# Kernel optimization log

Measured on AMD Instinct MI355X. Metric: run time of the kernel, lower is better.

## Reference

```python
import jax, jax.numpy as jnp
import numpy as np

B, N, IN, H, K, D, L = 8, 1024, 32, 32, 3, 16, 2  # batch, nodes, input_dim, hidden, cheb_k, embed_dim, layers


def setup_inputs() -> dict:
    key = jax.random.key(0)
    ks = jax.random.split(key, 4 + 4 * L)
    inp = {
        "xt": jax.random.normal(ks[0], (B, N, IN), jnp.float32),
        "init_state": jax.random.normal(ks[1], (L, B, N, H), jnp.float32),
        # row-normalized-ish support so the Chebyshev recursion stays bounded
        "support": jax.random.uniform(ks[2], (N, N), jnp.float32) / N,
        "embeddings": jax.random.normal(ks[3], (B, N, D), jnp.float32),
    }
    i = 4
    for l in range(L):
        cin = IN if l == 0 else H
        gi = K * (cin + H)
        inp[f"gate_w{l}"] = jax.random.normal(ks[i], (D, gi, 2 * H), jnp.float32) * (2.0 / (gi + 2 * H)) ** 0.5; i += 1
        inp[f"gate_b{l}"] = jax.random.normal(ks[i], (D, 2 * H), jnp.float32) * 0.05; i += 1
        inp[f"upd_w{l}"] = jax.random.normal(ks[i], (D, gi, H), jnp.float32) * (2.0 / (gi + H)) ** 0.5; i += 1
        inp[f"upd_b{l}"] = jax.random.normal(ks[i], (D, H), jnp.float32) * 0.05; i += 1
    return inp


def _cheb_gconv(x, support, emb, w_pool, b_pool):
    """HimGCN_share forward, meta_axis='ST', 2-D support.
    x: [B,N,C]; support: [N,N]; emb: [B,N,D];
    w_pool: [D, K*C, O]; b_pool: [D, O]. Returns [B,N,O]."""
    n = support.shape[0]
    graphs = [jnp.eye(n, dtype=x.dtype), support]
    for _ in range(2, K):
        graphs.append(2.0 * support @ graphs[-1] - graphs[-2])
    G = jnp.stack(graphs)                                   # [K,N,N]
    c = x.shape[-1]
    x_g = jnp.einsum('knm,bmc->bnkc', G, x).reshape(x.shape[0], n, K * c)  # concat over k
    # faithful to einsum('bni,bnio->bno') with bnio = einsum('bnd,dio->bnio'),
    # contracted in a memory-lighter order (same math)
    xe = jnp.einsum('bni,bnd->bnid', x_g, emb)              # [B,N,K*C,D]
    out = jnp.einsum('bnid,dio->bno', xe, w_pool)
    out = out + jnp.einsum('bnd,do->bno', emb, b_pool)
    return out


def _gcru_cell(x, state, support, emb, gw, gb, uw, ub):
    inp = jnp.concatenate([x, state], axis=-1)
    z_r = jax.nn.sigmoid(_cheb_gconv(inp, support, emb, gw, gb))
    z, r = z_r[..., :H], z_r[..., H:]
    cand = jnp.concatenate([x, z * state], axis=-1)
    hc = jnp.tanh(_cheb_gconv(cand, support, emb, uw, ub))
    return r * state + (1.0 - r) * hc


def reference(xt, init_state, support, embeddings,
              gate_w0, gate_b0, upd_w0, upd_b0,
              gate_w1, gate_b1, upd_w1, upd_b1):
    params = [(gate_w0, gate_b0, upd_w0, upd_b0), (gate_w1, gate_b1, upd_w1, upd_b1)]
    cur = xt
    hidden = []
    for l in range(L):
        gw, gb, uw, ub = params[l]
        cur = _gcru_cell(cur, init_state[l], support, embeddings, gw, gb, uw, ub)
        hidden.append(cur)
    return cur, jnp.stack(hidden)
```

## Files before the change

kernel.cpp:

```cpp
#include <hip/hip_runtime.h>
#include <math.h>

#define BB 8
#define NN 1024
#define HH 32
#define II 192
#define DD 16
#define BN (BB*NN)
#define MT 16
#define FR 512

typedef __attribute__((ext_vector_type(8))) short short8v;
typedef __attribute__((ext_vector_type(4))) float float4v;

union Frag8 { short8v v; uint2 u[2]; uint4 q; };

static __device__ inline ushort bf(float x) {
  union { float f; unsigned u; } c; c.f = x;
  unsigned r = c.u + 0x7FFFu + ((c.u >> 16) & 1u);
  return (ushort)(r >> 16);
}

static __device__ inline uint4 pack8(const ushort e[8]) {
  uint4 v;
  v.x = (unsigned)e[0] | ((unsigned)e[1] << 16);
  v.y = (unsigned)e[2] | ((unsigned)e[3] << 16);
  v.z = (unsigned)e[4] | ((unsigned)e[5] << 16);
  v.w = (unsigned)e[6] | ((unsigned)e[7] << 16);
  return v;
}

template <int O>
static __device__ void prep_w_frag(const float* __restrict__ W,
                                   ushort* __restrict__ WF, int d,
                                   float* lds)
{
  constexpr int NCG = O / 16;
  const float* Wd = W + (size_t)d * II * O;
  ushort* WFd = WF + (size_t)d * NCG * 6 * FR;
  const int tid = threadIdx.x;
  for (int f = tid; f < II * O / 4; f += 256) {
    int i = f / (O / 4);
    int o4 = (f % (O / 4)) * 4;
    float4 v = *(const float4*)(Wd + (size_t)i * O + o4);
    lds[i * (O + 1) + o4 + 0] = v.x; lds[i * (O + 1) + o4 + 1] = v.y;
    lds[i * (O + 1) + o4 + 2] = v.z; lds[i * (O + 1) + o4 + 3] = v.w;
  }
  __syncthreads();
  for (int f = tid; f < NCG * 6 * 64; f += 256) {
    int rem = f % 384;
    int ks = rem >> 6, l = rem & 63;
    int o = (f / 384) * 16 + (l & 15);
    int kb = ks * 32 + (l >> 4) * 4;
    ushort e[8];
#pragma unroll
    for (int j = 0; j < 4; ++j) {
      e[j] = bf(lds[(kb + j) * (O + 1) + o]);
      e[4 + j] = bf(lds[(kb + 16 + j) * (O + 1) + o]);
    }
    *(uint4*)(WFd + (size_t)f * 8) = pack8(e);
  }
}

__global__ __launch_bounds__(256) void prep_all(
    const float* __restrict__ S,
    ushort* __restrict__ SbF, ushort* __restrict__ S2bF,
    const float* __restrict__ gw0, const float* __restrict__ gw1,
    ushort* __restrict__ wfg0, ushort* __restrict__ wfg1,
    const float* __restrict__ uw0, const float* __restrict__ uw1,
    ushort* __restrict__ wfu0, ushort* __restrict__ wfu1,
    const float* __restrict__ xt, const float* __restrict__ st0,
    const float* __restrict__ st1,
    ushort* __restrict__ xbTFg0, ushort* __restrict__ xbTFg1)
{
  union PrepSm {
    float wlds[II * 65];
    struct { ushort A[32][136]; ushort Bt[32][132]; ushort C2[32][36]; } s2;
    ushort T[32 * 72];
  };
  __shared__ PrepSm sm;
  int bx = blockIdx.x;
  const int tid = threadIdx.x;

  if (bx < 1024) {
    const int m0 = (bx >> 5) * 32, n0 = (bx & 31) * 32;
    const int w = tid >> 6, l = tid & 63;
    const int l15 = l & 15, l4 = l >> 4;
    const int wr = (w & 1) * 16, wc = (w >> 1) * 16;

    float4v acc = (float4v){0.f, 0.f, 0.f, 0.f};
    for (int k0 = 0; k0 < NN; k0 += 128) {
      __syncthreads();
#pragma unroll
      for (int q = 0; q < 2; ++q) {
        int f = tid + q * 256;
        int row = f >> 4, s8 = (f & 15) * 8;
        float4 lo = *(const float4*)(S + (size_t)(m0 + row) * NN + k0 + s8);
        float4 hi = *(const float4*)(S + (size_t)(m0 + row) * NN + k0 + s8 + 4);
        sm.s2.A[row][s8 + 0] = bf(lo.x); sm.s2.A[row][s8 + 1] = bf(lo.y);
        sm.s2.A[row][s8 + 2] = bf(lo.z); sm.s2.A[row][s8 + 3] = bf(lo.w);
        sm.s2.A[row][s8 + 4] = bf(hi.x); sm.s2.A[row][s8 + 5] = bf(hi.y);
        sm.s2.A[row][s8 + 6] = bf(hi.z); sm.s2.A[row][s8 + 7] = bf(hi.w);
      }
#pragma unroll
      for (int q = 0; q < 2; ++q) {
        int u = tid + q * 256;
        int kp = u >> 3, c4 = (u & 7) * 4;
        float4 a = *(const float4*)(S + (size_t)(k0 + 2 * kp) * NN + n0 + c4);
        float4 b = *(const float4*)(S + (size_t)(k0 + 2 * kp + 1) * NN + n0 + c4);
        *(unsigned*)&sm.s2.Bt[c4 + 0][2 * kp] = (unsigned)bf(a.x) | ((unsigned)bf(b.x) << 16);
        *(unsigned*)&sm.s2.Bt[c4 + 1][2 * kp] = (unsigned)bf(a.y) | ((unsigned)bf(b.y) << 16);
        *(unsigned*)&sm.s2.Bt[c4 + 2][2 * kp] = (unsigned)bf(a.z) | ((unsigned)bf(b.z) << 16);
        *(unsigned*)&sm.s2.Bt[c4 + 3][2 * kp] = (unsigned)bf(a.w) | ((unsigned)bf(b.w) << 16);
      }
      __syncthreads();
#pragma unroll
      for (int ks = 0; ks < 4; ++ks) {
        int kb = ks * 32 + l4 * 4;
        Frag8 af, bfr;
        af.u[0] = *(const uint2*)&sm.s2.A[wr + l15][kb];
        af.u[1] = *(const uint2*)&sm.s2.A[wr + l15][kb + 16];
        bfr.u[0] = *(const uint2*)&sm.s2.Bt[wc + l15][kb];
        bfr.u[1] = *(const uint2*)&sm.s2.Bt[wc + l15][kb + 16];
        acc = __builtin_amdgcn_mfma_f32_16x16x32_bf16(af.v, bfr.v, acc, 0, 0, 0);
      }
    }
    __syncthreads();
#pragma unroll
    for (int r = 0; r < 4; ++r)
      sm.s2.C2[wr + l4 * 4 + r][wc + l15] = bf(2.f * acc[r]);
    __syncthreads();
    if (tid < 128) {
      int fh = tid >> 6, l2 = tid & 63;
      ushort e[8];
#pragma unroll
      for (int j = 0; j < 4; ++j) {
        e[j] = sm.s2.C2[fh * 16 + (l2 & 15)][(l2 >> 4) * 4 + j];
        e[4 + j] = sm.s2.C2[fh * 16 + (l2 & 15)][(l2 >> 4) * 4 + 16 + j];
      }
      *(uint4*)(S2bF + ((size_t)((bx >> 5) * 2 + fh) * 32 + (bx & 31)) * FR +
                (size_t)l2 * 8) = pack8(e);
    }
    return;
  }
  bx -= 1024;
  if (bx < 32) {
    prep_w_frag<64>(bx >= 16 ? gw1 : gw0, bx >= 16 ? wfg1 : wfg0, bx & 15,
                    sm.wlds);
    return;
  }
  bx -= 32;
  if (bx < 32) {
    prep_w_frag<32>(bx >= 16 ? uw1 : uw0, bx >= 16 ? wfu1 : wfu0, bx & 15,
                    sm.wlds);
    return;
  }
  bx -= 32;
  if (bx < 384) {
    const int tensor = bx / 128, seg = bx % 128;
    const float* src = tensor == 0 ? xt : (tensor == 1 ? st0 : st1);
    ushort* T = sm.T;
    const int n0 = seg * 64;
#pragma unroll
    for (int q = 0; q < 2; ++q) {
      int f = tid + q * 256;
      int n = f >> 3, c4 = (f & 7) * 4;
      float4 v = *(const float4*)(src + (size_t)(n0 + n) * 32 + c4);
      T[(c4 + 0) * 72 + n] = bf(v.x); T[(c4 + 1) * 72 + n] = bf(v.y);
      T[(c4 + 2) * 72 + n] = bf(v.z); T[(c4 + 3) * 72 + n] = bf(v.w);
    }
    __syncthreads();
    {
      int gg = tid >> 7, ksl = (tid >> 6) & 1, l = tid & 63;
      int c = gg * 16 + (l & 15);
      int nb = ksl * 32 + (l >> 4) * 4;
      ushort e[8];
#pragma unroll
      for (int j = 0; j < 4; ++j) {
        e[j] = T[c * 72 + nb + j];
        e[4 + j] = T[c * 72 + nb + 16 + j];
      }
      int b = seg >> 4;
      int ks = (seg & 15) * 2 + ksl;
      ushort* dst; int g;
      if (tensor == 0)      { dst = xbTFg0; g = gg; }
      else if (tensor == 1) { dst = xbTFg0; g = 2 + gg; }
      else                  { dst = xbTFg1; g = 2 + gg; }
      *(uint4*)(dst + (((size_t)b * 4 + g) * 32 + ks) * FR + (size_t)l * 8) =
          pack8(e);
    }
    return;
  }
  bx -= 384;
  {
    const int mt = bx;
#pragma unroll
    for (int q = 0; q < 8; ++q) {
      int f = tid + q * 256;
      int ks = f >> 6, l = f & 63;
      int row = mt * 16 + (l & 15);
      int kb = ks * 32 + (l >> 4) * 4;
      float4 lo = *(const float4*)(S + (size_t)row * NN + kb);
      float4 hi = *(const float4*)(S + (size_t)row * NN + kb + 16);
      ushort e[8] = {bf(lo.x), bf(lo.y), bf(lo.z), bf(lo.w),
                     bf(hi.x), bf(hi.y), bf(hi.z), bf(hi.w)};
      *(uint4*)(SbF + ((size_t)mt * 32 + ks) * FR + (size_t)l * 8) = pack8(e);
    }
  }
}

template <int PHASE>
__global__ __launch_bounds__(256) void gconv_fused(
    const float* __restrict__ xb1,
    const float* __restrict__ xb2,
    const ushort* __restrict__ xbTF,
    const ushort* __restrict__ SbF,
    const ushort* __restrict__ S2bF,
    const float* __restrict__ emb,
    const ushort* __restrict__ WF,
    const float* __restrict__ bias,
    ushort* __restrict__ gT1c,
    float* __restrict__ gT2c,
    float* __restrict__ zr,
    float* __restrict__ zs,
    const float* __restrict__ state,
    float* __restrict__ hid,
    float* __restrict__ outp,
    ushort* __restrict__ xbTFout)
{
  constexpr int O = PHASE == 0 ? 64 : 32;
  constexpr int NCG = O / 16;
  __shared__ ushort A_sm[MT][200];
  __shared__ float emb_sm[MT][17];
  __shared__ float bias_sm[16][64];

  const int bid = blockIdx.x;
  const int mt = (bid & 7) * 8 + ((bid >> 3) & 7);
  const int b = bid >> 6;
  const int m0 = mt * MT;
  const int tid = threadIdx.x;
  const int w = tid >> 6, l = tid & 63;
  const int l15 = l & 15, l4 = l >> 4;
  const int wcp = (PHASE == 0) ? w * 16 : (w & 1) * 16;

  if (tid < MT * 4) {
    int row = tid >> 2, d4 = (tid & 3) * 4;
    float4 v = *(const float4*)(emb + ((size_t)b * NN + m0 + row) * DD + d4);
    emb_sm[row][d4 + 0] = v.x; emb_sm[row][d4 + 1] = v.y;
    emb_sm[row][d4 + 2] = v.z; emb_sm[row][d4 + 3] = v.w;
  }
  for (int f = tid; f < DD * O / 4; f += 256) {
    int d = f / (O / 4), o4 = (f % (O / 4)) * 4;
    *(float4*)&bias_sm[d][o4] = *(const float4*)(bias + (size_t)d * O + o4);
  }
  {
    int row = tid >> 4, c4 = (tid & 15) * 4;
    const float* src = (c4 < 32) ? xb1 : xb2;
    float4 v = *(const float4*)(src + ((size_t)b * NN + m0 + row) * 32 + (c4 & 31));
    ushort4 o; o.x = bf(v.x); o.y = bf(v.y); o.z = bf(v.z); o.w = bf(v.w);
    *(ushort4*)&A_sm[row][c4] = o;
  }

  float4v acc1 = (float4v){0.f, 0.f, 0.f, 0.f};
  float4v acc2 = (float4v){0.f, 0.f, 0.f, 0.f};
  {
    const ushort* a1p = SbF + (size_t)mt * 32 * FR + (size_t)l * 8;
    const ushort* a2p = S2bF + (size_t)mt * 32 * FR + (size_t)l * 8;
    const ushort* bp = xbTF +
        (((size_t)b * NCG + (PHASE == 0 ? w : (w & 1))) * 32) * FR +
        (size_t)l * 8;
#pragma unroll 4
    for (int ks = 0; ks < 32; ++ks) {
      Frag8 a1, a2, b0;
      a1.q = *(const uint4*)(a1p + (size_t)ks * FR);
      a2.q = *(const uint4*)(a2p + (size_t)ks * FR);
      b0.q = *(const uint4*)(bp + (size_t)ks * FR);
      acc1 = __builtin_amdgcn_mfma_f32_16x16x32_bf16(a1.v, b0.v, acc1, 0, 0, 0);
      acc2 = __builtin_amdgcn_mfma_f32_16x16x32_bf16(a2.v, b0.v, acc2, 0, 0, 0);
    }
  }

  if (PHASE == 0 && w < 2) {
#pragma unroll
    for (int r = 0; r < 4; ++r) {
      size_t m = (size_t)b * NN + m0 + l4 * 4 + r;
      gT1c[m * 32 + wcp + l15] = bf(acc1[r]);
      gT2c[m * 32 + wcp + l15] = acc2[r];
    }
  }

  if (PHASE == 1) {
#pragma unroll
    for (int q = 0; q < 2; ++q) {
      int e = tid + q * 256;
      int row = e >> 5, c = e & 31;
      size_t m = (size_t)b * NN + m0 + row;
      A_sm[row][64 + c] = gT1c[m * 32 + c];
      A_sm[row][128 + c] = bf(gT2c[m * 32 + c] - xb1[m * 32 + c]);
    }
  }
  {
    const int colX = (PHASE == 0 ? 0 : 32) + wcp + l15;
    if (PHASE == 0 || w < 2) {
#pragma unroll
      for (int r = 0; r < 4; ++r) {
        int row = l4 * 4 + r;
        const float* src = (colX < 32) ? xb1 : xb2;
        float xv = src[((size_t)b * NN + m0 + row) * 32 + (colX & 31)];
        A_sm[row][64 + colX] = bf(acc1[r]);
        A_sm[row][128 + colX] = bf(acc2[r] - xv);
      }
    }
  }
  __syncthreads();

  const int cg = (PHASE == 0) ? w : (w & 1);
  const int ocol = cg * 16 + l15;
  const int erow = l4 * 4;
  const ushort* wfp = WF + (size_t)cg * 6 * FR + (size_t)l * 8;

  float4v outacc = (float4v){0.f, 0.f, 0.f, 0.f};

#pragma unroll 2
  for (int d = 0; d < DD; ++d) {
    const ushort* wpd = wfp + (size_t)d * NCG * 6 * FR;
    float4v acc = (float4v){0.f, 0.f, 0.f, 0.f};
#pragma unroll
    for (int ks = 0; ks < 6; ++ks) {
      int kb = ks * 32 + l4 * 4;
      Frag8 af, bfr;
      af.u[0] = *(const uint2*)&A_sm[l15][kb];
      af.u[1] = *(const uint2*)&A_sm[l15][kb + 16];
      bfr.q = *(const uint4*)(wpd + (size_t)ks * FR);
      acc = __builtin_amdgcn_mfma_f32_16x16x32_bf16(af.v, bfr.v, acc, 0, 0, 0);
    }
    float bb = bias_sm[d][ocol];
    outacc[0] += emb_sm[erow + 0][d] * (acc[0] + bb);
    outacc[1] += emb_sm[erow + 1][d] * (acc[1] + bb);
    outacc[2] += emb_sm[erow + 2][d] * (acc[2] + bb);
    outacc[3] += emb_sm[erow + 3][d] * (acc[3] + bb);
  }

  const int ksn = m0 >> 5;
  const int ebase = (m0 & 16) ? 4 : 0;
  const int lanep = l4 * 16 + (ocol & 15);

  if (PHASE == 0) {
    float zss[4];
#pragma unroll
    for (int r = 0; r < 4; ++r) {
      size_t m = (size_t)b * NN + m0 + erow + r;
      float zv = 1.f / (1.f + __expf(-outacc[r]));
      zr[m * 64 + ocol] = zv;
      if (ocol < 32) {
        float sv = zv * xb2[m * 32 + ocol];
        zs[m * 32 + ocol] = sv;
        zss[r] = sv;
      }
    }
    if (ocol < 32) {
      ushort4 pk; pk.x = bf(zss[0]); pk.y = bf(zss[1]);
      pk.z = bf(zss[2]); pk.w = bf(zss[3]);
      *(ushort4*)(xbTFout + (((size_t)b * 2 + (ocol >> 4)) * 32 + ksn) * FR +
                  (size_t)lanep * 8 + ebase) = pk;
    }
  } else if (w < 2) {
    float res[4];
#pragma unroll
    for (int r = 0; r < 4; ++r) {
      size_t m = (size_t)b * NN + m0 + erow + r;
      float hc = tanhf(outacc[r]);
      float rg = zr[m * 64 + 32 + ocol];
      float st = state[m * 32 + ocol];
      res[r] = rg * st + (1.f - rg) * hc;
      hid[m * 32 + ocol] = res[r];
      if (outp) outp[m * 32 + ocol] = res[r];
    }
    if (xbTFout) {
      ushort4 pk; pk.x = bf(res[0]); pk.y = bf(res[1]);
      pk.z = bf(res[2]); pk.w = bf(res[3]);
      *(ushort4*)(xbTFout + (((size_t)b * 4 + (ocol >> 4)) * 32 + ksn) * FR +
                  (size_t)lanep * 8 + ebase) = pk;
    }
  }
}

extern "C" void kernel_launch(void* const* d_in, const int* in_sizes, int n_in,
                              void* d_out, int out_size, void* d_ws, size_t ws_size,
                              hipStream_t stream)
{
  const float* xt         = (const float*)d_in[0];
  const float* init_state = (const float*)d_in[1];
  const float* S          = (const float*)d_in[2];
  const float* emb        = (const float*)d_in[3];

  float* out    = (float*)d_out;
  float* hidden = out + (size_t)BN * HH;

  float* zr   = (float*)d_ws;
  float* zs   = zr + (size_t)BN * 64;
  float* gT2c = zs + (size_t)BN * 32;
  ushort* gT1c = (ushort*)(gT2c + (size_t)BN * 32);
  ushort* SbF  = gT1c + (size_t)BN * 32;
  ushort* S2bF = SbF + (size_t)NN * NN;
  ushort* wfg0 = S2bF + (size_t)NN * NN;
  ushort* wfu0 = wfg0 + (size_t)DD * 4 * 6 * FR;
  ushort* wfg1 = wfu0 + (size_t)DD * 2 * 6 * FR;
  ushort* wfu1 = wfg1 + (size_t)DD * 4 * 6 * FR;
  ushort* xbTFg0 = wfu1 + (size_t)DD * 2 * 6 * FR;
  ushort* xbTFu0 = xbTFg0 + (size_t)BB * 4 * 32 * FR;
  ushort* xbTFg1 = xbTFu0 + (size_t)BB * 2 * 32 * FR;
  ushort* xbTFu1 = xbTFg1 + (size_t)BB * 4 * 32 * FR;

  const float* st0 = init_state;
  const float* st1 = init_state + (size_t)BN * HH;
  float* hid0 = hidden;
  float* hid1 = hidden + (size_t)BN * HH;

  prep_all<<<1536, 256, 0, stream>>>(
      S, SbF, S2bF,
      (const float*)d_in[4], (const float*)d_in[8], wfg0, wfg1,
      (const float*)d_in[6], (const float*)d_in[10], wfu0, wfu1,
      xt, st0, st1, xbTFg0, xbTFg1);

  gconv_fused<0><<<512, 256, 0, stream>>>(
      xt, st0, xbTFg0, SbF, S2bF, emb, wfg0, (const float*)d_in[5],
      gT1c, gT2c, zr, zs, nullptr, nullptr, nullptr, xbTFu0);
  gconv_fused<1><<<512, 256, 0, stream>>>(
      xt, zs, xbTFu0, SbF, S2bF, emb, wfu0, (const float*)d_in[7],
      gT1c, gT2c, zr, nullptr, st0, hid0, nullptr, xbTFg1);
  gconv_fused<0><<<512, 256, 0, stream>>>(
      hid0, st1, xbTFg1, SbF, S2bF, emb, wfg1, (const float*)d_in[9],
      gT1c, gT2c, zr, zs, nullptr, nullptr, nullptr, xbTFu1);
  gconv_fused<1><<<512, 256, 0, stream>>>(
      hid0, zs, xbTFu1, SbF, S2bF, emb, wfu1, (const float*)d_in[11],
      gT1c, gT2c, zr, nullptr, st1, hid1, out, nullptr);
}
```

Baseline: 99.87 us.

## Split-K gconv across two wave groups with LDS reduction, 512 threads

Doubles the block to 512 threads. The second group of four waves handles the other half of the K loop in the graph-propagation GEMM and the other half of the embedding dimension loop, and the partial results are reduced through a new shared-memory buffer. This halves the serial MFMA chain per wave and raises the number of waves in flight, since the grid has only 512 blocks. The cost is two extra barriers, more LDS traffic and larger shared-memory use per block. The phase-1 loads of gT1c/gT2c are also moved earlier so they overlap with the first GEMM.

Result: faster. 94.87 us (-5.0%).

```diff
diff --git a/kernel.cpp b/kernel.cpp
--- a/kernel.cpp
+++ b/kernel.cpp
@@ -210,7 +210,7 @@
 }
 
 template <int PHASE>
-__global__ __launch_bounds__(256) void gconv_fused(
+__global__ __launch_bounds__(512) void gconv_fused(
     const float* __restrict__ xb1,
     const float* __restrict__ xb2,
     const ushort* __restrict__ xbTF,
@@ -233,6 +233,7 @@
   __shared__ ushort A_sm[MT][200];
   __shared__ float emb_sm[MT][17];
   __shared__ float bias_sm[16][64];
+  __shared__ float red_sm[4][64][9];
 
   const int bid = blockIdx.x;
   const int mt = (bid & 7) * 8 + ((bid >> 3) & 7);
@@ -240,8 +241,9 @@
   const int m0 = mt * MT;
   const int tid = threadIdx.x;
   const int w = tid >> 6, l = tid & 63;
+  const int cw = w & 3, kh = w >> 2;
   const int l15 = l & 15, l4 = l >> 4;
-  const int wcp = (PHASE == 0) ? w * 16 : (w & 1) * 16;
+  const int wcp = (PHASE == 0) ? cw * 16 : (cw & 1) * 16;
 
   if (tid < MT * 4) {
     int row = tid >> 2, d4 = (tid & 3) * 4;
@@ -249,16 +251,22 @@
     emb_sm[row][d4 + 0] = v.x; emb_sm[row][d4 + 1] = v.y;
     emb_sm[row][d4 + 2] = v.z; emb_sm[row][d4 + 3] = v.w;
   }
-  for (int f = tid; f < DD * O / 4; f += 256) {
+  for (int f = tid; f < DD * O / 4; f += 512) {
     int d = f / (O / 4), o4 = (f % (O / 4)) * 4;
     *(float4*)&bias_sm[d][o4] = *(const float4*)(bias + (size_t)d * O + o4);
   }
-  {
+  if (tid < 256) {
     int row = tid >> 4, c4 = (tid & 15) * 4;
     const float* src = (c4 < 32) ? xb1 : xb2;
     float4 v = *(const float4*)(src + ((size_t)b * NN + m0 + row) * 32 + (c4 & 31));
     ushort4 o; o.x = bf(v.x); o.y = bf(v.y); o.z = bf(v.z); o.w = bf(v.w);
     *(ushort4*)&A_sm[row][c4] = o;
+  }
+  if (PHASE == 1) {
+    int row = tid >> 5, c = tid & 31;
+    size_t m = (size_t)b * NN + m0 + row;
+    A_sm[row][64 + c] = gT1c[m * 32 + c];
+    A_sm[row][128 + c] = bf(gT2c[m * 32 + c] - xb1[m * 32 + c]);
   }
 
   float4v acc1 = (float4v){0.f, 0.f, 0.f, 0.f};
@@ -267,10 +275,10 @@
     const ushort* a1p = SbF + (size_t)mt * 32 * FR + (size_t)l * 8;
     const ushort* a2p = S2bF + (size_t)mt * 32 * FR + (size_t)l * 8;
     const ushort* bp = xbTF +
-        (((size_t)b * NCG + (PHASE == 0 ? w : (w & 1))) * 32) * FR +
+        (((size_t)b * NCG + (PHASE == 0 ? cw : (cw & 1))) * 32) * FR +
         (size_t)l * 8;
 #pragma unroll 4
-    for (int ks = 0; ks < 32; ++ks) {
+    for (int ks = kh * 16; ks < kh * 16 + 16; ++ks) {
       Frag8 a1, a2, b0;
       a1.q = *(const uint4*)(a1p + (size_t)ks * FR);
       a2.q = *(const uint4*)(a2p + (size_t)ks * FR);
@@ -280,28 +288,30 @@
     }
   }
 
-  if (PHASE == 0 && w < 2) {
-#pragma unroll
-    for (int r = 0; r < 4; ++r) {
-      size_t m = (size_t)b * NN + m0 + l4 * 4 + r;
-      gT1c[m * 32 + wcp + l15] = bf(acc1[r]);
-      gT2c[m * 32 + wcp + l15] = acc2[r];
-    }
-  }
-
-  if (PHASE == 1) {
-#pragma unroll
-    for (int q = 0; q < 2; ++q) {
-      int e = tid + q * 256;
-      int row = e >> 5, c = e & 31;
-      size_t m = (size_t)b * NN + m0 + row;
-      A_sm[row][64 + c] = gT1c[m * 32 + c];
-      A_sm[row][128 + c] = bf(gT2c[m * 32 + c] - xb1[m * 32 + c]);
-    }
-  }
-  {
-    const int colX = (PHASE == 0 ? 0 : 32) + wcp + l15;
-    if (PHASE == 0 || w < 2) {
+  if (kh == 1) {
+#pragma unroll
+    for (int j = 0; j < 4; ++j) {
+      red_sm[cw][l][j] = acc1[j];
+      red_sm[cw][l][4 + j] = acc2[j];
+    }
+  }
+  __syncthreads();
+  if (kh == 0) {
+#pragma unroll
+    for (int j = 0; j < 4; ++j) {
+      acc1[j] += red_sm[cw][l][j];
+      acc2[j] += red_sm[cw][l][4 + j];
+    }
+    if (PHASE == 0 && cw < 2) {
+#pragma unroll
+      for (int r = 0; r < 4; ++r) {
+        size_t m = (size_t)b * NN + m0 + l4 * 4 + r;
+        gT1c[m * 32 + wcp + l15] = bf(acc1[r]);
+        gT2c[m * 32 + wcp + l15] = acc2[r];
+      }
+    }
+    if (PHASE == 0 || cw < 2) {
+      const int colX = (PHASE == 0 ? 0 : 32) + wcp + l15;
 #pragma unroll
       for (int r = 0; r < 4; ++r) {
         int row = l4 * 4 + r;
@@ -314,7 +324,7 @@
   }
   __syncthreads();
 
-  const int cg = (PHASE == 0) ? w : (w & 1);
+  const int cg = (PHASE == 0) ? cw : (cw & 1);
   const int ocol = cg * 16 + l15;
   const int erow = l4 * 4;
   const ushort* wfp = WF + (size_t)cg * 6 * FR + (size_t)l * 8;
@@ -322,7 +332,7 @@
   float4v outacc = (float4v){0.f, 0.f, 0.f, 0.f};
 
 #pragma unroll 2
-  for (int d = 0; d < DD; ++d) {
+  for (int d = kh * 8; d < kh * 8 + 8; ++d) {
     const ushort* wpd = wfp + (size_t)d * NCG * 6 * FR;
     float4v acc = (float4v){0.f, 0.f, 0.f, 0.f};
 #pragma unroll
@@ -340,6 +350,15 @@
     outacc[2] += emb_sm[erow + 2][d] * (acc[2] + bb);
     outacc[3] += emb_sm[erow + 3][d] * (acc[3] + bb);
   }
+
+  if (kh == 1) {
+#pragma unroll
+    for (int j = 0; j < 4; ++j) red_sm[cw][l][j] = outacc[j];
+  }
+  __syncthreads();
+  if (kh != 0) return;
+#pragma unroll
+  for (int j = 0; j < 4; ++j) outacc[j] += red_sm[cw][l][j];
 
   const int ksn = m0 >> 5;
   const int ebase = (m0 & 16) ? 4 : 0;
@@ -364,7 +383,7 @@
       *(ushort4*)(xbTFout + (((size_t)b * 2 + (ocol >> 4)) * 32 + ksn) * FR +
                   (size_t)lanep * 8 + ebase) = pk;
     }
-  } else if (w < 2) {
+  } else if (cw < 2) {
     float res[4];
 #pragma unroll
     for (int r = 0; r < 4; ++r) {
@@ -423,16 +442,16 @@
       (const float*)d_in[6], (const float*)d_in[10], wfu0, wfu1,
       xt, st0, st1, xbTFg0, xbTFg1);
 
-  gconv_fused<0><<<512, 256, 0, stream>>>(
+  gconv_fused<0><<<512, 512, 0, stream>>>(
       xt, st0, xbTFg0, SbF, S2bF, emb, wfg0, (const float*)d_in[5],
       gT1c, gT2c, zr, zs, nullptr, nullptr, nullptr, xbTFu0);
-  gconv_fused<1><<<512, 256, 0, stream>>>(
+  gconv_fused<1><<<512, 512, 0, stream>>>(
       xt, zs, xbTFu0, SbF, S2bF, emb, wfu0, (const float*)d_in[7],
       gT1c, gT2c, zr, nullptr, st0, hid0, nullptr, xbTFg1);
-  gconv_fused<0><<<512, 256, 0, stream>>>(
+  gconv_fused<0><<<512, 512, 0, stream>>>(
       hid0, st1, xbTFg1, SbF, S2bF, emb, wfg1, (const float*)d_in[9],
       gT1c, gT2c, zr, zs, nullptr, nullptr, nullptr, xbTFu1);
-  gconv_fused<1><<<512, 256, 0, stream>>>(
+  gconv_fused<1><<<512, 512, 0, stream>>>(
       hid0, zs, xbTFu1, SbF, S2bF, emb, wfu1, (const float*)d_in[11],
       gT1c, gT2c, zr, nullptr, st1, hid1, out, nullptr);
 }
```
